# Optimization experiments

Measured on AMD Instinct MI355X. Metric: run time of the kernel, lower is better.

## Reference

```python
import jax, jax.numpy as jnp
import numpy as np


def _lstm_layer(x, h0, c0, w_ih, w_hh, b):
    """x: [T,B,I], h0/c0: [B,H], w_ih: [4H,I], w_hh: [4H,H], b: [4H]. PyTorch gate order i,f,g,o."""
    H = h0.shape[-1]
    # Precompute input projection for all timesteps in one big GEMM.
    xg = jnp.einsum('tbi,gi->tbg', x, w_ih) + b  # [T,B,4H]

    def step(carry, xg_t):
        h, c = carry
        g = xg_t + h @ w_hh.T  # [B,4H]
        i, f, gg, o = jnp.split(g, 4, axis=-1)
        c_new = jax.nn.sigmoid(f) * c + jax.nn.sigmoid(i) * jnp.tanh(gg)
        h_new = jax.nn.sigmoid(o) * jnp.tanh(c_new)
        return (h_new, c_new), h_new

    (_, _), hs = jax.lax.scan(step, (h0, c0), xg)
    return hs  # [T,B,H]


def setup_inputs() -> dict:
    key = jax.random.key(0)
    ks = jax.random.split(key, 12)
    T, B, I, H, O, L = 2048, 32, 256, 512, 1024, 2
    s = 1.0 / np.sqrt(H)  # PyTorch LSTM init scale
    return {
        'x': jax.random.normal(ks[0], (T, B, I), jnp.float32),
        'h0': jnp.zeros((L, B, H), jnp.float32),
        'c0': jnp.zeros((L, B, H), jnp.float32),
        'w_ih0': jax.random.normal(ks[1], (4 * H, I), jnp.float32) * s,
        'w_hh0': jax.random.normal(ks[2], (4 * H, H), jnp.float32) * s,
        'b_ih0': jax.random.normal(ks[3], (4 * H,), jnp.float32) * s,
        'b_hh0': jax.random.normal(ks[4], (4 * H,), jnp.float32) * s,
        'w_ih1': jax.random.normal(ks[5], (4 * H, H), jnp.float32) * s,
        'w_hh1': jax.random.normal(ks[6], (4 * H, H), jnp.float32) * s,
        'b_ih1': jax.random.normal(ks[7], (4 * H,), jnp.float32) * s,
        'b_hh1': jax.random.normal(ks[8], (4 * H,), jnp.float32) * s,
        'fc_w': jax.random.normal(ks[9], (O, H), jnp.float32) * s,
        'fc_b': jax.random.normal(ks[10], (O,), jnp.float32) * s,
    }


def reference(x, h0, c0, w_ih0, w_hh0, b_ih0, b_hh0, w_ih1, w_hh1, b_ih1, b_hh1, fc_w, fc_b):
    h1 = _lstm_layer(x, h0[0], c0[0], w_ih0, w_hh0, b_ih0 + b_hh0)   # [T,B,H]
    h2 = _lstm_layer(h1, h0[1], c0[1], w_ih1, w_hh1, b_ih1 + b_hh1)  # [T,B,H]
    logits = h2[-1] @ fc_w.T + fc_b  # out[-1] -> fc, [B,O]
    return jax.nn.log_softmax(logits, axis=1)
```

## Files before the change

### kernel.cpp

```cpp
#include <hip/hip_runtime.h>
#include <stdint.h>

#define TT 2048
#define BB 32
#define II 256
#define HH 512
#define OO 1024
#define NWGL 64
#define NWG 128

typedef __attribute__((ext_vector_type(8))) short short8;
typedef __attribute__((ext_vector_type(4))) float floatx4;

__device__ __forceinline__ unsigned short f2bf(float f) {
  union { float f; unsigned u; } v; v.f = f;
  unsigned r = v.u + 0x7FFFu + ((v.u >> 16) & 1u);
  return (unsigned short)(r >> 16);
}
__device__ __forceinline__ float bf2f(unsigned short b) {
  union { float f; unsigned u; } v; v.u = ((unsigned)b) << 16; return v.f;
}
__device__ __forceinline__ float sigmf(float x) { return 1.0f / (1.0f + __expf(-x)); }
__device__ __forceinline__ float tanhfast(float x) {
  float xc = fminf(fmaxf(x, -15.f), 15.f);
  float e = __expf(2.f * xc);
  return (e - 1.f) / (e + 1.f);
}

#define LD1(d, va, IMM)                                                     \
  asm volatile("global_load_dwordx4 %0, %1, off offset:" IMM " sc0 sc1"     \
               : "=v"(d) : "v"(va) : "memory")

#define ISSUE8(dst, va) do {                                                \
    LD1(dst[0], va, "0");   LD1(dst[1], va, "64");                          \
    LD1(dst[2], va, "128"); LD1(dst[3], va, "192");                         \
    LD1(dst[4], va, "256"); LD1(dst[5], va, "320");                         \
    LD1(dst[6], va, "384"); LD1(dst[7], va, "448"); } while (0)

#define WAITV(N) do {                                                       \
    asm volatile("s_waitcnt vmcnt(" #N ")" ::: "memory");                   \
    __builtin_amdgcn_sched_barrier(0); } while (0)

#define MF8(tt_, src, wbase) do {                                           \
    _Pragma("unroll")                                                       \
    for (int j = 0; j < 8; j++) {                                           \
      acc[0][tt_] = __builtin_amdgcn_mfma_f32_16x16x32_bf16(src[j], wf[0][(wbase) + j], acc[0][tt_], 0, 0, 0); \
      acc[1][tt_] = __builtin_amdgcn_mfma_f32_16x16x32_bf16(src[j], wf[1][(wbase) + j], acc[1][tt_], 0, 0, 0); \
    } } while (0)

__global__ void k_convert_x(const float* __restrict__ x, ushort* __restrict__ xb, int n4) {
  int i = blockIdx.x * blockDim.x + threadIdx.x;
  int stride = gridDim.x * blockDim.x;
  const float4* xf = reinterpret_cast<const float4*>(x);
  ushort4* ob = reinterpret_cast<ushort4*>(xb);
  for (; i < n4; i += stride) {
    float4 f = xf[i];
    ushort4 o;
    o.x = f2bf(f.x); o.y = f2bf(f.y); o.z = f2bf(f.z); o.w = f2bf(f.w);
    ob[i] = o;
  }
}

__global__ void k_init(const float* __restrict__ h0in, ushort* __restrict__ h0b1,
                       ushort* __restrict__ h1b1, int* __restrict__ bar) {
  int i = threadIdx.x;
  for (int k = i; k < BB * HH; k += blockDim.x) {
    h0b1[k] = f2bf(h0in[k]);
    h1b1[k] = f2bf(h0in[BB * HH + k]);
  }
  for (int k = i; k < 1024; k += blockDim.x) bar[k] = 0;
}

__global__ __launch_bounds__(64, 1) void k_lstm(
    const ushort* __restrict__ xb,
    const float* __restrict__ w_ih0, const float* __restrict__ w_hh0,
    const float* __restrict__ b_ih0, const float* __restrict__ b_hh0,
    const float* __restrict__ w_ih1, const float* __restrict__ w_hh1,
    const float* __restrict__ b_ih1, const float* __restrict__ b_hh1,
    const float* __restrict__ c0in,
    ushort* __restrict__ h0b0, ushort* __restrict__ h0b1,
    ushort* __restrict__ h1b0, ushort* __restrict__ h1b1,
    int* __restrict__ bar)
{
  __shared__ ushort sh[BB][8];
  const int wg = blockIdx.x;
  const int lane = threadIdx.x;
  const bool isL0 = wg < NWGL;
  const int g = isL0 ? wg : wg - NWGL;
  const int col = lane & 15;
  const int krow = lane >> 4;
  const int u = col & 3;
  const int gate = col >> 2;

  short8 wf[2][32];
#define LOADW(dst, base, rowlen, kbase, tau) do {                             \
    const int _grow = gate * HH + g * 8 + (tau) * 4 + u;                      \
    const float* _p = (base) + (size_t)_grow * (rowlen) + (kbase) + krow * 8; \
    short8 _r;                                                                \
    _Pragma("unroll")                                                         \
    for (int _j = 0; _j < 8; _j++) _r[_j] = (short)f2bf(_p[_j]);              \
    (dst) = _r; } while (0)

  if (isL0) {
#pragma unroll
    for (int tau = 0; tau < 2; tau++) {
#pragma unroll
      for (int kk = 0; kk < 8; kk++)  LOADW(wf[tau][kk],      w_ih0, II, kk * 32, tau);
#pragma unroll
      for (int kk = 0; kk < 16; kk++) LOADW(wf[tau][8 + kk],  w_hh0, HH, kk * 32, tau);
    }
  } else {
#pragma unroll
    for (int tau = 0; tau < 2; tau++) {
#pragma unroll
      for (int kk = 0; kk < 16; kk++) LOADW(wf[tau][kk],      w_ih1, HH, kk * 32, tau);
#pragma unroll
      for (int kk = 0; kk < 16; kk++) LOADW(wf[tau][16 + kk], w_hh1, HH, kk * 32, tau);
    }
  }
  float bias[2];
#pragma unroll
  for (int tau = 0; tau < 2; tau++) {
    const int grow = gate * HH + g * 8 + tau * 4 + u;
    bias[tau] = isL0 ? (b_ih0[grow] + b_hh0[grow]) : (b_ih1[grow] + b_hh1[grow]);
  }

  float cst[2][2][4];
  {
    const float* cbase = c0in + (isL0 ? 0 : 1) * BB * HH;
#pragma unroll
    for (int tau = 0; tau < 2; tau++)
#pragma unroll
      for (int tt = 0; tt < 2; tt++)
#pragma unroll
        for (int r = 0; r < 4; r++) {
          int b = tt * 16 + krow * 4 + r;
          cst[tau][tt][r] = cbase[b * HH + g * 8 + tau * 4 + u];
        }
  }

  ushort* h0bufs[2] = { h0b0, h0b1 };
  ushort* h1bufs[2] = { h1b0, h1b1 };
  int* gcnt = bar + (wg >> 4) * 32;
  int* root = bar + 512;
  int* gen  = bar + 544;

  const int vo00 = col * 1024 + krow * 16;
  const unsigned long long stoff = (unsigned long long)(lane * 1024 + g * 16);

  const int P = TT + 1;
  for (int p = 0; p < P; ++p) {
    const bool active = isL0 ? (p < TT) : (p >= 1);
    if (active) {
      floatx4 acc[2][2];
#pragma unroll
      for (int tau = 0; tau < 2; tau++) {
        floatx4 bi = (floatx4){ bias[tau], bias[tau], bias[tau], bias[tau] };
        acc[tau][0] = bi; acc[tau][1] = bi;
      }
      short8 wa[8], wb[8];
      if (isL0) {
        const ushort* xr = xb + (size_t)p * BB * II;
#pragma unroll
        for (int tt = 0; tt < 2; tt++) {
          const int b = tt * 16 + col;
#pragma unroll
          for (int kk = 0; kk < 8; kk++) {
            short8 a = *reinterpret_cast<const short8*>(xr + b * II + kk * 32 + krow * 8);
            acc[0][tt] = __builtin_amdgcn_mfma_f32_16x16x32_bf16(a, wf[0][kk], acc[0][tt], 0, 0, 0);
            acc[1][tt] = __builtin_amdgcn_mfma_f32_16x16x32_bf16(a, wf[1][kk], acc[1][tt], 0, 0, 0);
          }
        }
        const unsigned long long ha = (unsigned long long)h0bufs[(p + 1) & 1] + vo00;
        ISSUE8(wa, ha);
        ISSUE8(wb, ha + 512);
        WAITV(8);  MF8(0, wa, 8);
        ISSUE8(wa, ha + 16384);
        WAITV(8);  MF8(0, wb, 16);
        ISSUE8(wb, ha + 16896);
        WAITV(8);  MF8(1, wa, 8);
        WAITV(0);  MF8(1, wb, 16);
      } else {
        const int t = p - 1;
        const unsigned long long a0 = (unsigned long long)h0bufs[t & 1] + vo00;
        const unsigned long long a1 = (unsigned long long)h1bufs[(t + 1) & 1] + vo00;
        ISSUE8(wa, a0);
        ISSUE8(wb, a0 + 512);
        WAITV(8);  MF8(0, wa, 0);
        ISSUE8(wa, a0 + 16384);
        WAITV(8);  MF8(0, wb, 8);
        ISSUE8(wb, a0 + 16896);
        WAITV(8);  MF8(1, wa, 0);
        ISSUE8(wa, a1);
        WAITV(8);  MF8(1, wb, 8);
        ISSUE8(wb, a1 + 512);
        WAITV(8);  MF8(0, wa, 16);
        ISSUE8(wa, a1 + 16384);
        WAITV(8);  MF8(0, wb, 24);
        ISSUE8(wb, a1 + 16896);
        WAITV(8);  MF8(1, wa, 16);
        WAITV(0);  MF8(1, wb, 24);
      }
      ushort* hw = isL0 ? h0bufs[p & 1] : h1bufs[(p - 1) & 1];
#pragma unroll
      for (int tau = 0; tau < 2; tau++) {
#pragma unroll
        for (int tt = 0; tt < 2; tt++) {
#pragma unroll
          for (int r = 0; r < 4; r++) {
            float val = acc[tau][tt][r];
            float nl = (gate == 2) ? tanhfast(val) : sigmf(val);
            int base2 = (lane & 48) | u;
            float iv = __shfl(nl, base2);
            float fv = __shfl(nl, base2 | 4);
            float gv = __shfl(nl, base2 | 8);
            float ov = __shfl(nl, base2 | 12);
            if (gate == 0) {
              float cn = fv * cst[tau][tt][r] + iv * gv;
              cst[tau][tt][r] = cn;
              float hn = ov * tanhfast(cn);
              int b = tt * 16 + krow * 4 + r;
              sh[b][tau * 4 + u] = f2bf(hn);
            }
          }
        }
      }
      asm volatile("s_waitcnt lgkmcnt(0)" ::: "memory");
      __builtin_amdgcn_sched_barrier(0);
      if (lane < 32) {
        short8 v = *reinterpret_cast<const short8*>(&sh[lane][0]);
        unsigned long long sa = (unsigned long long)hw + stoff;
        asm volatile("global_store_dwordx4 %0, %1, off sc0 sc1"
                     :: "v"(sa), "v"(v) : "memory");
      }
    }
    if (p != P - 1) {
      asm volatile("s_waitcnt vmcnt(0)" ::: "memory");
      if (lane == 0) {
        const int target = p + 1;
        int prev = __hip_atomic_fetch_add(gcnt, 1, __ATOMIC_RELAXED, __HIP_MEMORY_SCOPE_AGENT);
        if (prev == 16 * target - 1) {
          int p2 = __hip_atomic_fetch_add(root, 1, __ATOMIC_RELAXED, __HIP_MEMORY_SCOPE_AGENT);
          if (p2 == 8 * target - 1) {
            __hip_atomic_store(gen, target, __ATOMIC_RELAXED, __HIP_MEMORY_SCOPE_AGENT);
          } else {
            while (__hip_atomic_load(gen, __ATOMIC_RELAXED, __HIP_MEMORY_SCOPE_AGENT) < target)
              __builtin_amdgcn_s_sleep(1);
          }
        } else {
          while (__hip_atomic_load(gen, __ATOMIC_RELAXED, __HIP_MEMORY_SCOPE_AGENT) < target)
            __builtin_amdgcn_s_sleep(1);
        }
      }
    }
  }
}

__global__ __launch_bounds__(256) void k_fc(const ushort* __restrict__ h1,
                                            const float* __restrict__ fcw,
                                            const float* __restrict__ fcb,
                                            float* __restrict__ out) {
  __shared__ float hsh[HH];
  __shared__ float red[256];
  const int b = blockIdx.x, tid = threadIdx.x;
  for (int k = tid; k < HH; k += 256) hsh[k] = bf2f(h1[b * HH + k]);
  __syncthreads();
  float lg[4];
#pragma unroll
  for (int q = 0; q < 4; q++) {
    int o = q * 256 + tid;
    float acc = fcb[o];
    const float* wr = fcw + (size_t)o * HH;
#pragma unroll 4
    for (int k = 0; k < HH; k += 4) {
      float4 w4 = *reinterpret_cast<const float4*>(wr + k);
      acc += hsh[k] * w4.x + hsh[k + 1] * w4.y + hsh[k + 2] * w4.z + hsh[k + 3] * w4.w;
    }
    lg[q] = acc;
  }
  float m = fmaxf(fmaxf(lg[0], lg[1]), fmaxf(lg[2], lg[3]));
  red[tid] = m; __syncthreads();
  for (int s = 128; s > 0; s >>= 1) { if (tid < s) red[tid] = fmaxf(red[tid], red[tid + s]); __syncthreads(); }
  m = red[0]; __syncthreads();
  float se = 0.f;
#pragma unroll
  for (int q = 0; q < 4; q++) se += __expf(lg[q] - m);
  red[tid] = se; __syncthreads();
  for (int s = 128; s > 0; s >>= 1) { if (tid < s) red[tid] += red[tid + s]; __syncthreads(); }
  float lse = m + logf(red[0]);
#pragma unroll
  for (int q = 0; q < 4; q++) out[b * OO + q * 256 + tid] = lg[q] - lse;
}

extern "C" void kernel_launch(void* const* d_in, const int* in_sizes, int n_in,
                              void* d_out, int out_size, void* d_ws, size_t ws_size,
                              hipStream_t stream) {
  const float* x     = (const float*)d_in[0];
  const float* h0    = (const float*)d_in[1];
  const float* c0    = (const float*)d_in[2];
  const float* w_ih0 = (const float*)d_in[3];
  const float* w_hh0 = (const float*)d_in[4];
  const float* b_ih0 = (const float*)d_in[5];
  const float* b_hh0 = (const float*)d_in[6];
  const float* w_ih1 = (const float*)d_in[7];
  const float* w_hh1 = (const float*)d_in[8];
  const float* b_ih1 = (const float*)d_in[9];
  const float* b_hh1 = (const float*)d_in[10];
  const float* fcw   = (const float*)d_in[11];
  const float* fcb   = (const float*)d_in[12];
  float* out = (float*)d_out;

  char* ws = (char*)d_ws;
  size_t off = 0;
  ushort* xb = (ushort*)(ws + off); off += (size_t)TT * BB * II * 2;
  ushort* h0b0 = (ushort*)(ws + off); off += BB * HH * 2;
  ushort* h0b1 = (ushort*)(ws + off); off += BB * HH * 2;
  ushort* h1b0 = (ushort*)(ws + off); off += BB * HH * 2;
  ushort* h1b1 = (ushort*)(ws + off); off += BB * HH * 2;
  int* bar = (int*)(ws + off); off += 1024 * sizeof(int);

  k_convert_x<<<2048, 256, 0, stream>>>(x, xb, TT * BB * II / 4);
  k_init<<<1, 256, 0, stream>>>(h0, h0b1, h1b1, bar);
  k_lstm<<<NWG, 64, 0, stream>>>(xb, w_ih0, w_hh0, b_ih0, b_hh0,
                                 w_ih1, w_hh1, b_ih1, b_hh1, c0,
                                 h0b0, h0b1, h1b0, h1b1, bar);
  k_fc<<<BB, 256, 0, stream>>>(h1b1, fcw, fcb, out);
}
```

Before: 17.63 ms.

## Decouple LSTM layers with separate barriers and a ring buffer for layer-0 hidden states

Replaces the single 128-workgroup grid barrier shared by both layers with two independent per-layer barriers. Layer 0 writes its hidden states into a 32-slot ring, so it can run ahead of layer 1 and throttles only when it gets about 24 steps ahead. Layer 1 polls layer 0's generation counter before reading. Layer 1 also issues its own recurrent loads before waiting on layer 0, and layer 0 loads x through a non-coherent path overlapped with the recurrent MFMAs. The aim is to remove lockstep coupling and shrink per-step barrier fan-in, at the cost of extra cross-layer polling and a more complex memory-ordering scheme.

```diff
diff --git a/kernel.cpp b/kernel.cpp
--- a/kernel.cpp
+++ b/kernel.cpp
@@ -8,6 +8,7 @@
 #define OO 1024
 #define NWGL 64
 #define NWG 128
+#define RING 32
 
 typedef __attribute__((ext_vector_type(8))) short short8;
 typedef __attribute__((ext_vector_type(4))) float floatx4;
@@ -30,12 +31,20 @@
 #define LD1(d, va, IMM)                                                     \
   asm volatile("global_load_dwordx4 %0, %1, off offset:" IMM " sc0 sc1"     \
                : "=v"(d) : "v"(va) : "memory")
+#define LD1C(d, va, IMM)                                                    \
+  asm volatile("global_load_dwordx4 %0, %1, off offset:" IMM                \
+               : "=v"(d) : "v"(va) : "memory")
 
 #define ISSUE8(dst, va) do {                                                \
     LD1(dst[0], va, "0");   LD1(dst[1], va, "64");                          \
     LD1(dst[2], va, "128"); LD1(dst[3], va, "192");                         \
     LD1(dst[4], va, "256"); LD1(dst[5], va, "320");                         \
     LD1(dst[6], va, "384"); LD1(dst[7], va, "448"); } while (0)
+#define ISSUE8C(dst, va) do {                                               \
+    LD1C(dst[0], va, "0");   LD1C(dst[1], va, "64");                        \
+    LD1C(dst[2], va, "128"); LD1C(dst[3], va, "192");                       \
+    LD1C(dst[4], va, "256"); LD1C(dst[5], va, "320");                       \
+    LD1C(dst[6], va, "384"); LD1C(dst[7], va, "448"); } while (0)
 
 #define WAITV(N) do {                                                       \
     asm volatile("s_waitcnt vmcnt(" #N ")" ::: "memory");                   \
@@ -47,6 +56,60 @@
       acc[0][tt_] = __builtin_amdgcn_mfma_f32_16x16x32_bf16(src[j], wf[0][(wbase) + j], acc[0][tt_], 0, 0, 0); \
       acc[1][tt_] = __builtin_amdgcn_mfma_f32_16x16x32_bf16(src[j], wf[1][(wbase) + j], acc[1][tt_], 0, 0, 0); \
     } } while (0)
+
+#define PROGREAD(dst, addr64)                                               \
+  asm volatile("global_load_dword %0, %1, off sc0 sc1"                      \
+               : "=v"(dst) : "v"(addr64) : "memory")
+
+#define BARRIER(gcnt, root, gen, target, do_poll) do {                      \
+  if (lane == 0) {                                                          \
+    int prev = __hip_atomic_fetch_add(gcnt, 1, __ATOMIC_RELAXED, __HIP_MEMORY_SCOPE_AGENT); \
+    if (prev == 8 * (target) - 1) {                                         \
+      int p2 = __hip_atomic_fetch_add(root, 1, __ATOMIC_RELAXED, __HIP_MEMORY_SCOPE_AGENT); \
+      if (p2 == 8 * (target) - 1) {                                         \
+        __hip_atomic_store(gen, (target), __ATOMIC_RELAXED, __HIP_MEMORY_SCOPE_AGENT); \
+      } else if (do_poll) {                                                 \
+        while (__hip_atomic_load(gen, __ATOMIC_RELAXED, __HIP_MEMORY_SCOPE_AGENT) < (target)) \
+          __builtin_amdgcn_s_sleep(1);                                      \
+      }                                                                     \
+    } else if (do_poll) {                                                   \
+      while (__hip_atomic_load(gen, __ATOMIC_RELAXED, __HIP_MEMORY_SCOPE_AGENT) < (target)) \
+        __builtin_amdgcn_s_sleep(1);                                        \
+    }                                                                       \
+  } } while (0)
+
+#define TAIL(hwaddr) do {                                                   \
+  _Pragma("unroll")                                                         \
+  for (int tau = 0; tau < 2; tau++) {                                       \
+    _Pragma("unroll")                                                       \
+    for (int tt = 0; tt < 2; tt++) {                                        \
+      _Pragma("unroll")                                                     \
+      for (int r = 0; r < 4; r++) {                                         \
+        float val = acc[tau][tt][r];                                        \
+        float nl = (gate == 2) ? tanhfast(val) : sigmf(val);                \
+        int base2 = (lane & 48) | u;                                        \
+        float iv = __shfl(nl, base2);                                       \
+        float fv = __shfl(nl, base2 | 4);                                   \
+        float gv = __shfl(nl, base2 | 8);                                   \
+        float ov = __shfl(nl, base2 | 12);                                  \
+        if (gate == 0) {                                                    \
+          float cn = fv * cst[tau][tt][r] + iv * gv;                        \
+          cst[tau][tt][r] = cn;                                             \
+          float hn = ov * tanhfast(cn);                                     \
+          int b = tt * 16 + krow * 4 + r;                                   \
+          sh[b][tau * 4 + u] = f2bf(hn);                                    \
+        }                                                                   \
+      }                                                                     \
+    }                                                                       \
+  }                                                                         \
+  asm volatile("s_waitcnt lgkmcnt(0)" ::: "memory");                        \
+  __builtin_amdgcn_sched_barrier(0);                                        \
+  if (lane < 32) {                                                          \
+    short8 v = *reinterpret_cast<const short8*>(&sh[lane][0]);              \
+    unsigned long long sa = (hwaddr) + stoff;                               \
+    asm volatile("global_store_dwordx4 %0, %1, off sc0 sc1"                 \
+                 :: "v"(sa), "v"(v) : "memory");                            \
+  } } while (0)
 
 __global__ void k_convert_x(const float* __restrict__ x, ushort* __restrict__ xb, int n4) {
   int i = blockIdx.x * blockDim.x + threadIdx.x;
@@ -61,12 +124,13 @@
   }
 }
 
-__global__ void k_init(const float* __restrict__ h0in, ushort* __restrict__ h0b1,
+__global__ void k_init(const float* __restrict__ h0in, ushort* __restrict__ ring,
                        ushort* __restrict__ h1b1, int* __restrict__ bar) {
   int i = threadIdx.x;
+  ushort* slot31 = ring + (RING - 1) * BB * HH;
   for (int k = i; k < BB * HH; k += blockDim.x) {
-    h0b1[k] = f2bf(h0in[k]);
-    h1b1[k] = f2bf(h0in[BB * HH + k]);
+    slot31[k] = f2bf(h0in[k]);
+    h1b1[k]   = f2bf(h0in[BB * HH + k]);
   }
   for (int k = i; k < 1024; k += blockDim.x) bar[k] = 0;
 }
@@ -78,7 +142,7 @@
     const float* __restrict__ w_ih1, const float* __restrict__ w_hh1,
     const float* __restrict__ b_ih1, const float* __restrict__ b_hh1,
     const float* __restrict__ c0in,
-    ushort* __restrict__ h0b0, ushort* __restrict__ h0b1,
+    ushort* __restrict__ ring,
     ushort* __restrict__ h1b0, ushort* __restrict__ h1b1,
     int* __restrict__ bar)
 {
@@ -139,119 +203,79 @@
         }
   }
 
-  ushort* h0bufs[2] = { h0b0, h0b1 };
-  ushort* h1bufs[2] = { h1b0, h1b1 };
-  int* gcnt = bar + (wg >> 4) * 32;
-  int* root = bar + 512;
-  int* gen  = bar + 544;
+  int* gcnt = bar + (isL0 ? 0 : 320) + (g >> 3) * 32;
+  int* root = bar + (isL0 ? 256 : 576);
+  int* gen  = bar + (isL0 ? 288 : 608);
+  const unsigned long long genOther =
+      (unsigned long long)(bar + (isL0 ? 608 : 288));
 
   const int vo00 = col * 1024 + krow * 16;
   const unsigned long long stoff = (unsigned long long)(lane * 1024 + g * 16);
-
-  const int P = TT + 1;
-  for (int p = 0; p < P; ++p) {
-    const bool active = isL0 ? (p < TT) : (p >= 1);
-    if (active) {
-      floatx4 acc[2][2];
-#pragma unroll
-      for (int tau = 0; tau < 2; tau++) {
-        floatx4 bi = (floatx4){ bias[tau], bias[tau], bias[tau], bias[tau] };
-        acc[tau][0] = bi; acc[tau][1] = bi;
-      }
-      short8 wa[8], wb[8];
-      if (isL0) {
-        const ushort* xr = xb + (size_t)p * BB * II;
-#pragma unroll
-        for (int tt = 0; tt < 2; tt++) {
-          const int b = tt * 16 + col;
-#pragma unroll
-          for (int kk = 0; kk < 8; kk++) {
-            short8 a = *reinterpret_cast<const short8*>(xr + b * II + kk * 32 + krow * 8);
-            acc[0][tt] = __builtin_amdgcn_mfma_f32_16x16x32_bf16(a, wf[0][kk], acc[0][tt], 0, 0, 0);
-            acc[1][tt] = __builtin_amdgcn_mfma_f32_16x16x32_bf16(a, wf[1][kk], acc[1][tt], 0, 0, 0);
-          }
-        }
-        const unsigned long long ha = (unsigned long long)h0bufs[(p + 1) & 1] + vo00;
-        ISSUE8(wa, ha);
-        ISSUE8(wb, ha + 512);
-        WAITV(8);  MF8(0, wa, 8);
-        ISSUE8(wa, ha + 16384);
-        WAITV(8);  MF8(0, wb, 16);
-        ISSUE8(wb, ha + 16896);
-        WAITV(8);  MF8(1, wa, 8);
-        WAITV(0);  MF8(1, wb, 16);
-      } else {
-        const int t = p - 1;
-        const unsigned long long a0 = (unsigned long long)h0bufs[t & 1] + vo00;
-        const unsigned long long a1 = (unsigned long long)h1bufs[(t + 1) & 1] + vo00;
-        ISSUE8(wa, a0);
-        ISSUE8(wb, a0 + 512);
-        WAITV(8);  MF8(0, wa, 0);
-        ISSUE8(wa, a0 + 16384);
-        WAITV(8);  MF8(0, wb, 8);
-        ISSUE8(wb, a0 + 16896);
-        WAITV(8);  MF8(1, wa, 0);
-        ISSUE8(wa, a1);
-        WAITV(8);  MF8(1, wb, 8);
-        ISSUE8(wb, a1 + 512);
-        WAITV(8);  MF8(0, wa, 16);
-        ISSUE8(wa, a1 + 16384);
-        WAITV(8);  MF8(0, wb, 24);
-        ISSUE8(wb, a1 + 16896);
-        WAITV(8);  MF8(1, wa, 16);
-        WAITV(0);  MF8(1, wb, 24);
-      }
-      ushort* hw = isL0 ? h0bufs[p & 1] : h1bufs[(p - 1) & 1];
-#pragma unroll
-      for (int tau = 0; tau < 2; tau++) {
-#pragma unroll
-        for (int tt = 0; tt < 2; tt++) {
-#pragma unroll
-          for (int r = 0; r < 4; r++) {
-            float val = acc[tau][tt][r];
-            float nl = (gate == 2) ? tanhfast(val) : sigmf(val);
-            int base2 = (lane & 48) | u;
-            float iv = __shfl(nl, base2);
-            float fv = __shfl(nl, base2 | 4);
-            float gv = __shfl(nl, base2 | 8);
-            float ov = __shfl(nl, base2 | 12);
-            if (gate == 0) {
-              float cn = fv * cst[tau][tt][r] + iv * gv;
-              cst[tau][tt][r] = cn;
-              float hn = ov * tanhfast(cn);
-              int b = tt * 16 + krow * 4 + r;
-              sh[b][tau * 4 + u] = f2bf(hn);
-            }
-          }
+  ushort* h1bufs[2] = { h1b0, h1b1 };
+
+  short8 wa[8], wb[8], wc[8], wd[8];
+  floatx4 acc[2][2];
+  const floatx4 bi0 = (floatx4){ bias[0], bias[0], bias[0], bias[0] };
+  const floatx4 bi1 = (floatx4){ bias[1], bias[1], bias[1], bias[1] };
+
+  if (isL0) {
+    const unsigned long long xbase = (unsigned long long)xb + (col * 512 + krow * 16);
+    int seen1 = 0;
+    for (int t = 0; t < TT; ++t) {
+      if (((t & 7) == 0) && t >= 32) {
+        while (seen1 < t - 24) {
+          int sv; PROGREAD(sv, genOther); WAITV(0); seen1 = sv;
+          if (seen1 < t - 24) __builtin_amdgcn_s_sleep(8);
         }
       }
-      asm volatile("s_waitcnt lgkmcnt(0)" ::: "memory");
-      __builtin_amdgcn_sched_barrier(0);
-      if (lane < 32) {
-        short8 v = *reinterpret_cast<const short8*>(&sh[lane][0]);
-        unsigned long long sa = (unsigned long long)hw + stoff;
-        asm volatile("global_store_dwordx4 %0, %1, off sc0 sc1"
-                     :: "v"(sa), "v"(v) : "memory");
-      }
-    }
-    if (p != P - 1) {
-      asm volatile("s_waitcnt vmcnt(0)" ::: "memory");
-      if (lane == 0) {
-        const int target = p + 1;
-        int prev = __hip_atomic_fetch_add(gcnt, 1, __ATOMIC_RELAXED, __HIP_MEMORY_SCOPE_AGENT);
-        if (prev == 16 * target - 1) {
-          int p2 = __hip_atomic_fetch_add(root, 1, __ATOMIC_RELAXED, __HIP_MEMORY_SCOPE_AGENT);
-          if (p2 == 8 * target - 1) {
-            __hip_atomic_store(gen, target, __ATOMIC_RELAXED, __HIP_MEMORY_SCOPE_AGENT);
-          } else {
-            while (__hip_atomic_load(gen, __ATOMIC_RELAXED, __HIP_MEMORY_SCOPE_AGENT) < target)
-              __builtin_amdgcn_s_sleep(1);
-          }
-        } else {
-          while (__hip_atomic_load(gen, __ATOMIC_RELAXED, __HIP_MEMORY_SCOPE_AGENT) < target)
-            __builtin_amdgcn_s_sleep(1);
+      acc[0][0] = bi0; acc[0][1] = bi0; acc[1][0] = bi1; acc[1][1] = bi1;
+      const unsigned long long ha =
+          (unsigned long long)ring + ((t + RING - 1) & (RING - 1)) * (BB * HH * 2) + vo00;
+      const unsigned long long xa = xbase + (unsigned long long)t * (BB * II * 2);
+      ISSUE8(wa, ha); ISSUE8(wb, ha + 512); ISSUE8(wc, ha + 16384); ISSUE8(wd, ha + 16896);
+      WAITV(24); MF8(0, wa, 8);  ISSUE8C(wa, xa);
+      WAITV(24); MF8(0, wb, 16); ISSUE8C(wb, xa + 8192);
+      WAITV(24); MF8(1, wc, 8);
+      WAITV(16); MF8(1, wd, 16);
+      WAITV(8);  MF8(0, wa, 0);
+      WAITV(0);  MF8(1, wb, 0);
+      const unsigned long long hw =
+          (unsigned long long)ring + (t & (RING - 1)) * (BB * HH * 2);
+      TAIL(hw);
+      WAITV(0);
+      BARRIER(gcnt, root, gen, t + 1, (t != TT - 1));
+    }
+  } else {
+    int seen0 = 0;
+    int sv_next = 0;
+    for (int t = 0; t < TT; ++t) {
+      acc[0][0] = bi0; acc[0][1] = bi0; acc[1][0] = bi1; acc[1][1] = bi1;
+      const unsigned long long h1a =
+          (unsigned long long)h1bufs[(t + 1) & 1] + vo00;
+      ISSUE8(wa, h1a); ISSUE8(wb, h1a + 512); ISSUE8(wc, h1a + 16384); ISSUE8(wd, h1a + 16896);
+      if (seen0 < t + 1) {
+        while (true) {
+          int sv; PROGREAD(sv, genOther); WAITV(0); seen0 = sv;
+          if (seen0 >= t + 1) break;
+          __builtin_amdgcn_s_sleep(8);
         }
       }
+      const unsigned long long h0a =
+          (unsigned long long)ring + (t & (RING - 1)) * (BB * HH * 2) + vo00;
+      WAITV(24); MF8(0, wa, 16); ISSUE8(wa, h0a);
+      WAITV(24); MF8(0, wb, 24); ISSUE8(wb, h0a + 512);
+      WAITV(24); MF8(1, wc, 16); ISSUE8(wc, h0a + 16384);
+      WAITV(24); MF8(1, wd, 24); ISSUE8(wd, h0a + 16896);
+      WAITV(24); MF8(0, wa, 0);
+      WAITV(16); MF8(0, wb, 8);
+      WAITV(8);  MF8(1, wc, 0);
+      WAITV(0);  MF8(1, wd, 8);
+      const unsigned long long hw = (unsigned long long)h1bufs[t & 1];
+      TAIL(hw);
+      PROGREAD(sv_next, genOther);
+      WAITV(0);
+      seen0 = (sv_next > seen0) ? sv_next : seen0;
+      if (t != TT - 1) BARRIER(gcnt, root, gen, t + 1, true);
     }
   }
 }
@@ -312,17 +336,16 @@
 
   char* ws = (char*)d_ws;
   size_t off = 0;
-  ushort* xb = (ushort*)(ws + off); off += (size_t)TT * BB * II * 2;
-  ushort* h0b0 = (ushort*)(ws + off); off += BB * HH * 2;
-  ushort* h0b1 = (ushort*)(ws + off); off += BB * HH * 2;
+  ushort* xb   = (ushort*)(ws + off); off += (size_t)TT * BB * II * 2;
+  ushort* ring = (ushort*)(ws + off); off += (size_t)RING * BB * HH * 2;
   ushort* h1b0 = (ushort*)(ws + off); off += BB * HH * 2;
   ushort* h1b1 = (ushort*)(ws + off); off += BB * HH * 2;
   int* bar = (int*)(ws + off); off += 1024 * sizeof(int);
 
   k_convert_x<<<2048, 256, 0, stream>>>(x, xb, TT * BB * II / 4);
-  k_init<<<1, 256, 0, stream>>>(h0, h0b1, h1b1, bar);
+  k_init<<<1, 256, 0, stream>>>(h0, ring, h1b1, bar);
   k_lstm<<<NWG, 64, 0, stream>>>(xb, w_ih0, w_hh0, b_ih0, b_hh0,
                                  w_ih1, w_hh1, b_ih1, b_hh1, c0,
-                                 h0b0, h0b1, h1b0, h1b1, bar);
+                                 ring, h1b0, h1b1, bar);
   k_fc<<<BB, 256, 0, stream>>>(h1b1, fcw, fcb, out);
 }
```

Measured after the change: 16.12 ms. 1.09x faster.
